# Kernel optimization log

Hardware: AMD Instinct MI355X
Metric: run time of the kernel (lower is better)

The kernel has to match this reference:

```python
import jax, jax.numpy as jnp
import numpy as np

N_NODES = 50000
N_EDGES = 800000
D_IN = 512
D_OUT = 256

def setup_inputs() -> dict:
    key = jax.random.key(0)
    k1, k2, k3, k4, k5 = jax.random.split(key, 5)
    return {
        "inputs": jax.random.normal(k1, (N_NODES, D_IN), dtype=jnp.float32),
        "weights": jax.random.uniform(k2, (D_IN, D_OUT), dtype=jnp.float32, minval=-0.1, maxval=0.1),
        "bias": jnp.zeros((D_OUT,), dtype=jnp.float32),
        "edge_vals": jax.random.uniform(k3, (N_EDGES,), dtype=jnp.float32),
        "edge_row": jax.random.randint(k4, (N_EDGES,), 0, N_NODES),
        "edge_col": jax.random.randint(k5, (N_EDGES,), 0, N_NODES),
    }

def reference(inputs, weights, bias, edge_vals, edge_row, edge_col):
    # dense projection: [N, D_in] @ [D_in, D_out] -> [N, D_out]
    supports = inputs @ weights
    # sparse adjacency spmm in COO form: out[i] = sum_e vals[e] * supports[col[e]] for row[e] == i
    msgs = supports[edge_col] * edge_vals[:, None]  # [E, D_out]
    aggregated = jax.ops.segment_sum(msgs, edge_row, num_segments=inputs.shape[0])
    return aggregated + bias
```

## Files before the change

### kernel.cpp

```cpp
#include <hip/hip_runtime.h>

#define D_IN 512
#define D_OUT 256
#define BM 128
#define BN 128
#define BK 32
#define LDK 40

#define HIST_BLOCKS 1563
#define GEMM_MTILES 391
#define GEMM_BLOCKS (GEMM_MTILES * 2)

typedef short short8 __attribute__((ext_vector_type(8)));
typedef float floatx4 __attribute__((ext_vector_type(4)));

static __device__ __forceinline__ unsigned short f2bf(float f) {
    unsigned u = __float_as_uint(f);
    u += 0x7FFF + ((u >> 16) & 1);
    return (unsigned short)(u >> 16);
}
static __device__ __forceinline__ float bf2f(unsigned short h) {
    return __uint_as_float((unsigned)h << 16);
}

__global__ __launch_bounds__(256) void prep(const float* __restrict__ W,
                                            unsigned short* __restrict__ Wt,
                                            int* __restrict__ cnt, int M) {
    int b = blockIdx.x;
    if (b < 512) {
        int t = b * 256 + threadIdx.x;
        int n = t >> 9;
        int k = t & 511;
        Wt[t] = f2bf(W[(size_t)k * D_OUT + n]);
    } else {
        int i = (b - 512) * 256 + threadIdx.x;
        if (i < M) cnt[i] = 0;
    }
}

__global__ __launch_bounds__(512) void gemm_hist(const float* __restrict__ A,
                                                 const unsigned short* __restrict__ Wt,
                                                 unsigned short* __restrict__ S,
                                                 const int* __restrict__ rows,
                                                 int* __restrict__ cnt, int M, int E) {
    if (blockIdx.x < HIST_BLOCKS) {
        int e = blockIdx.x * 512 + threadIdx.x;
        if (e < E) atomicAdd(&cnt[rows[e]], 1);
        return;
    }
    const int gb = blockIdx.x - HIST_BLOCKS;
    const int bm = (gb >> 1) * BM;
    const int bn = (gb & 1) * BN;

    __shared__ unsigned short As[BM * LDK];
    __shared__ unsigned short Bs[BN * LDK];
    const int tid  = threadIdx.x;
    const int lane = tid & 63;
    const int wave = tid >> 6;
    const int wm   = (wave >> 2) * 64;
    const int wn   = (wave & 3) * 32;
    const int l15  = lane & 15;
    const int quad = lane >> 4;

    const float* aptr[2];
    const unsigned short* bptr[2];
    int aoff[2], boff[2];
    bool aval[2];
#pragma unroll
    for (int i = 0; i < 2; ++i) {
        int item = tid + i * 512;
        int m  = item >> 3;
        int k4 = (item & 7) * 4;
        int gm = bm + m;
        aval[i] = gm < M;
        aptr[i] = A + (size_t)(aval[i] ? gm : 0) * D_IN + k4;
        aoff[i] = m * LDK + k4;
        bptr[i] = Wt + (size_t)(bn + m) * D_IN + k4;
        boff[i] = m * LDK + k4;
    }

    float4  aR[2];
    ushort4 bR[2];
#pragma unroll
    for (int i = 0; i < 2; ++i) {
        aR[i] = aval[i] ? *(const float4*)(aptr[i]) : make_float4(0.f, 0.f, 0.f, 0.f);
        bR[i] = *(const ushort4*)(bptr[i]);
    }

    floatx4 acc[4][2] = {};

    for (int k0 = 0; k0 < D_IN; k0 += BK) {
#pragma unroll
        for (int i = 0; i < 2; ++i) {
            ushort4 b;
            b.x = f2bf(aR[i].x); b.y = f2bf(aR[i].y);
            b.z = f2bf(aR[i].z); b.w = f2bf(aR[i].w);
            *(ushort4*)(As + aoff[i]) = b;
            *(ushort4*)(Bs + boff[i]) = bR[i];
        }
        __syncthreads();

        if (k0 + BK < D_IN) {
#pragma unroll
            for (int i = 0; i < 2; ++i) {
                aR[i] = aval[i] ? *(const float4*)(aptr[i] + k0 + BK)
                                : make_float4(0.f, 0.f, 0.f, 0.f);
                bR[i] = *(const ushort4*)(bptr[i] + k0 + BK);
            }
        }

        short8 af[4], bfr[2];
#pragma unroll
        for (int i = 0; i < 4; ++i)
            af[i] = *(const short8*)(As + (wm + i * 16 + l15) * LDK + quad * 8);
#pragma unroll
        for (int j = 0; j < 2; ++j)
            bfr[j] = *(const short8*)(Bs + (wn + j * 16 + l15) * LDK + quad * 8);
#pragma unroll
        for (int i = 0; i < 4; ++i)
#pragma unroll
            for (int j = 0; j < 2; ++j)
                acc[i][j] = __builtin_amdgcn_mfma_f32_16x16x32_bf16(
                    af[i], bfr[j], acc[i][j], 0, 0, 0);
        __syncthreads();
    }

#pragma unroll
    for (int i = 0; i < 4; ++i) {
#pragma unroll
        for (int r = 0; r < 4; ++r) {
            int gm = bm + wm + i * 16 + quad * 4 + r;
            if (gm < M) {
#pragma unroll
                for (int j = 0; j < 2; ++j)
                    S[(size_t)gm * D_OUT + bn + wn + j * 16 + l15] = f2bf(acc[i][j][r]);
            }
        }
    }
}

__global__ __launch_bounds__(1024) void scan_rowptr(const int* __restrict__ cnt,
                                                    int* __restrict__ ptr,
                                                    int* __restrict__ fill, int M) {
    __shared__ int wsum[16];
    __shared__ int sh_carry;
    const int t = threadIdx.x, lane = t & 63, wave = t >> 6;
    if (t == 0) sh_carry = 0;
    __syncthreads();
    for (int base0 = 0; base0 < M; base0 += 4096) {
        int base = base0 + t * 4;
        int4 v = make_int4(0, 0, 0, 0);
        if (base + 3 < M) v = *(const int4*)(cnt + base);
        else {
            if (base + 0 < M) v.x = cnt[base + 0];
            if (base + 1 < M) v.y = cnt[base + 1];
            if (base + 2 < M) v.z = cnt[base + 2];
        }
        int s = v.x + v.y + v.z + v.w;
        int incl = s;
#pragma unroll
        for (int off = 1; off < 64; off <<= 1) {
            int x = __shfl_up(incl, off, 64);
            if (lane >= off) incl += x;
        }
        if (lane == 63) wsum[wave] = incl;
        __syncthreads();
        if (t == 0) {
            int run = sh_carry;
#pragma unroll
            for (int w = 0; w < 16; ++w) { int x = wsum[w]; wsum[w] = run; run += x; }
            sh_carry = run;
        }
        __syncthreads();
        int e0 = wsum[wave] + (incl - s);
        int e1 = e0 + v.x, e2 = e1 + v.y, e3 = e2 + v.z;
        if (base + 3 < M) {
            *(int4*)(ptr + base)  = make_int4(e0, e1, e2, e3);
            *(int4*)(fill + base) = make_int4(e0, e1, e2, e3);
        } else {
            if (base + 0 < M) { ptr[base + 0] = e0; fill[base + 0] = e0; }
            if (base + 1 < M) { ptr[base + 1] = e1; fill[base + 1] = e1; }
            if (base + 2 < M) { ptr[base + 2] = e2; fill[base + 2] = e2; }
        }
        __syncthreads();
    }
    if (t == 0) ptr[M] = sh_carry;
}

__global__ __launch_bounds__(256) void build_sorted(const float* __restrict__ vals,
                                                    const int* __restrict__ rows,
                                                    const int* __restrict__ cols,
                                                    int* __restrict__ fill,
                                                    int2* __restrict__ edges, int E) {
    int e = blockIdx.x * 256 + threadIdx.x;
    if (e >= E) return;
    int pos = atomicAdd(&fill[rows[e]], 1);
    edges[pos] = make_int2(cols[e], __float_as_int(vals[e]));
}

__global__ __launch_bounds__(256) void spmm_rows(const unsigned short* __restrict__ S,
                                                 const int2* __restrict__ edges,
                                                 const int* __restrict__ ptr,
                                                 const float* __restrict__ bias,
                                                 float* __restrict__ out, int M) {
    const int row = blockIdx.x * 4 + (threadIdx.x >> 6);
    if (row >= M) return;
    const int lane = threadIdx.x & 63;
    float4 a0 = ((const float4*)bias)[lane];
    float4 a1 = make_float4(0.f, 0.f, 0.f, 0.f);
    float4 a2 = make_float4(0.f, 0.f, 0.f, 0.f);
    float4 a3 = make_float4(0.f, 0.f, 0.f, 0.f);
    const int beg = ptr[row];
    const int end = ptr[row + 1];
    int j = beg;
    const int end8 = beg + ((end - beg) & ~7);
    for (; j < end8; j += 8) {
        int4 p01 = *(const int4*)(edges + j);
        int4 p23 = *(const int4*)(edges + j + 2);
        int4 p45 = *(const int4*)(edges + j + 4);
        int4 p67 = *(const int4*)(edges + j + 6);
        ushort4 s0 = ((const ushort4*)(S + (size_t)p01.x * D_OUT))[lane];
        ushort4 s1 = ((const ushort4*)(S + (size_t)p01.z * D_OUT))[lane];
        ushort4 s2 = ((const ushort4*)(S + (size_t)p23.x * D_OUT))[lane];
        ushort4 s3 = ((const ushort4*)(S + (size_t)p23.z * D_OUT))[lane];
        ushort4 s4 = ((const ushort4*)(S + (size_t)p45.x * D_OUT))[lane];
        ushort4 s5 = ((const ushort4*)(S + (size_t)p45.z * D_OUT))[lane];
        ushort4 s6 = ((const ushort4*)(S + (size_t)p67.x * D_OUT))[lane];
        ushort4 s7 = ((const ushort4*)(S + (size_t)p67.z * D_OUT))[lane];
        float v0 = __int_as_float(p01.y), v1 = __int_as_float(p01.w);
        float v2 = __int_as_float(p23.y), v3 = __int_as_float(p23.w);
        float v4 = __int_as_float(p45.y), v5 = __int_as_float(p45.w);
        float v6 = __int_as_float(p67.y), v7 = __int_as_float(p67.w);
        a0.x += v0 * bf2f(s0.x) + v4 * bf2f(s4.x);
        a0.y += v0 * bf2f(s0.y) + v4 * bf2f(s4.y);
        a0.z += v0 * bf2f(s0.z) + v4 * bf2f(s4.z);
        a0.w += v0 * bf2f(s0.w) + v4 * bf2f(s4.w);
        a1.x += v1 * bf2f(s1.x) + v5 * bf2f(s5.x);
        a1.y += v1 * bf2f(s1.y) + v5 * bf2f(s5.y);
        a1.z += v1 * bf2f(s1.z) + v5 * bf2f(s5.z);
        a1.w += v1 * bf2f(s1.w) + v5 * bf2f(s5.w);
        a2.x += v2 * bf2f(s2.x) + v6 * bf2f(s6.x);
        a2.y += v2 * bf2f(s2.y) + v6 * bf2f(s6.y);
        a2.z += v2 * bf2f(s2.z) + v6 * bf2f(s6.z);
        a2.w += v2 * bf2f(s2.w) + v6 * bf2f(s6.w);
        a3.x += v3 * bf2f(s3.x) + v7 * bf2f(s7.x);
        a3.y += v3 * bf2f(s3.y) + v7 * bf2f(s7.y);
        a3.z += v3 * bf2f(s3.z) + v7 * bf2f(s7.z);
        a3.w += v3 * bf2f(s3.w) + v7 * bf2f(s7.w);
    }
    if (j + 3 < end) {
        int4 p01 = *(const int4*)(edges + j);
        int4 p23 = *(const int4*)(edges + j + 2);
        ushort4 s0 = ((const ushort4*)(S + (size_t)p01.x * D_OUT))[lane];
        ushort4 s1 = ((const ushort4*)(S + (size_t)p01.z * D_OUT))[lane];
        ushort4 s2 = ((const ushort4*)(S + (size_t)p23.x * D_OUT))[lane];
        ushort4 s3 = ((const ushort4*)(S + (size_t)p23.z * D_OUT))[lane];
        float v0 = __int_as_float(p01.y), v1 = __int_as_float(p01.w);
        float v2 = __int_as_float(p23.y), v3 = __int_as_float(p23.w);
        a0.x += v0 * bf2f(s0.x) + v2 * bf2f(s2.x);
        a0.y += v0 * bf2f(s0.y) + v2 * bf2f(s2.y);
        a0.z += v0 * bf2f(s0.z) + v2 * bf2f(s2.z);
        a0.w += v0 * bf2f(s0.w) + v2 * bf2f(s2.w);
        a1.x += v1 * bf2f(s1.x) + v3 * bf2f(s3.x);
        a1.y += v1 * bf2f(s1.y) + v3 * bf2f(s3.y);
        a1.z += v1 * bf2f(s1.z) + v3 * bf2f(s3.z);
        a1.w += v1 * bf2f(s1.w) + v3 * bf2f(s3.w);
        j += 4;
    }
    for (; j < end; ++j) {
        int2 e = edges[j];
        float v = __int_as_float(e.y);
        ushort4 s = ((const ushort4*)(S + (size_t)e.x * D_OUT))[lane];
        a0.x += v * bf2f(s.x);
        a0.y += v * bf2f(s.y);
        a0.z += v * bf2f(s.z);
        a0.w += v * bf2f(s.w);
    }
    a0.x += a1.x + a2.x + a3.x;
    a0.y += a1.y + a2.y + a3.y;
    a0.z += a1.z + a2.z + a3.z;
    a0.w += a1.w + a2.w + a3.w;
    ((float4*)out)[(size_t)row * 64 + lane] = a0;
}

extern "C" void kernel_launch(void* const* d_in, const int* in_sizes, int n_in,
                              void* d_out, int out_size, void* d_ws, size_t ws_size,
                              hipStream_t stream) {
    const float* inputs    = (const float*)d_in[0];
    const float* weights   = (const float*)d_in[1];
    const float* bias      = (const float*)d_in[2];
    const float* edge_vals = (const float*)d_in[3];
    const int*   edge_row  = (const int*)d_in[4];
    const int*   edge_col  = (const int*)d_in[5];
    float* out = (float*)d_out;

    const int M = in_sizes[0] / D_IN;
    const int E = in_sizes[3];

    char* ws = (char*)d_ws;
    unsigned short* S  = (unsigned short*)ws;
    unsigned short* Wt = (unsigned short*)(ws + (size_t)M * D_OUT * 2);
    int2* edges        = (int2*)((char*)Wt + (size_t)D_OUT * D_IN * 2);
    int*  ptr          = (int*)((char*)edges + (size_t)E * 8);
    int*  cnt          = ptr + ((M + 4) & ~3);
    int*  fill         = cnt + ((M + 4) & ~3);

    prep<<<512 + (M + 255) / 256, 256, 0, stream>>>(weights, Wt, cnt, M);

    gemm_hist<<<HIST_BLOCKS + GEMM_BLOCKS, 512, 0, stream>>>(inputs, Wt, S, edge_row,
                                                             cnt, M, E);

    scan_rowptr<<<1, 1024, 0, stream>>>(cnt, ptr, fill, M);

    build_sorted<<<(E + 255) / 256, 256, 0, stream>>>(edge_vals, edge_row, edge_col,
                                                      fill, edges, E);

    spmm_rows<<<(M + 3) / 4, 256, 0, stream>>>(S, edges, ptr, bias, out, M);
}
```

Before: 342.5 us.

## Restructure GEMM to stream A from registers and split histogram into own kernel

The GEMM now has each wave own 16 rows and all 128 columns. A values are loaded from global memory directly into registers and converted to bf16 there, so only B is staged in LDS, in 64-wide K chunks. The edge-row histogram is moved out of the fused kernel into a separate kernel that uses int4 loads and four atomics per thread. This removes the A staging traffic through LDS and half the barriers, at the cost of uncoalesced, non-reused A loads and one extra kernel launch. The new histogram also drops the remainder edges when E is not a multiple of 4.

```diff
diff --git a/kernel.cpp b/kernel.cpp
--- a/kernel.cpp
+++ b/kernel.cpp
@@ -2,14 +2,6 @@
 
 #define D_IN 512
 #define D_OUT 256
-#define BM 128
-#define BN 128
-#define BK 32
-#define LDK 40
-
-#define HIST_BLOCKS 1563
-#define GEMM_MTILES 391
-#define GEMM_BLOCKS (GEMM_MTILES * 2)
 
 typedef short short8 __attribute__((ext_vector_type(8)));
 typedef float floatx4 __attribute__((ext_vector_type(4)));
@@ -38,104 +30,76 @@
     }
 }
 
-__global__ __launch_bounds__(512) void gemm_hist(const float* __restrict__ A,
+#define LDB 72
+__global__ __launch_bounds__(512) void gemm_bf16(const float* __restrict__ A,
                                                  const unsigned short* __restrict__ Wt,
-                                                 unsigned short* __restrict__ S,
-                                                 const int* __restrict__ rows,
-                                                 int* __restrict__ cnt, int M, int E) {
-    if (blockIdx.x < HIST_BLOCKS) {
-        int e = blockIdx.x * 512 + threadIdx.x;
-        if (e < E) atomicAdd(&cnt[rows[e]], 1);
-        return;
-    }
-    const int gb = blockIdx.x - HIST_BLOCKS;
-    const int bm = (gb >> 1) * BM;
-    const int bn = (gb & 1) * BN;
-
-    __shared__ unsigned short As[BM * LDK];
-    __shared__ unsigned short Bs[BN * LDK];
+                                                 unsigned short* __restrict__ S, int M) {
+    __shared__ unsigned short Bs[128 * LDB];
     const int tid  = threadIdx.x;
     const int lane = tid & 63;
-    const int wave = tid >> 6;
-    const int wm   = (wave >> 2) * 64;
-    const int wn   = (wave & 3) * 32;
+    const int w    = tid >> 6;
     const int l15  = lane & 15;
     const int quad = lane >> 4;
-
-    const float* aptr[2];
-    const unsigned short* bptr[2];
-    int aoff[2], boff[2];
-    bool aval[2];
+    const int bm   = blockIdx.x * 128;
+    const int bn   = blockIdx.y * 128;
+    const int row  = bm + w * 16 + l15;
+    const float* arow = A + (size_t)(row < M ? row : 0) * D_IN;
+
+    int sn[2], sk[2];
 #pragma unroll
     for (int i = 0; i < 2; ++i) {
-        int item = tid + i * 512;
-        int m  = item >> 3;
-        int k4 = (item & 7) * 4;
-        int gm = bm + m;
-        aval[i] = gm < M;
-        aptr[i] = A + (size_t)(aval[i] ? gm : 0) * D_IN + k4;
-        aoff[i] = m * LDK + k4;
-        bptr[i] = Wt + (size_t)(bn + m) * D_IN + k4;
-        boff[i] = m * LDK + k4;
-    }
-
-    float4  aR[2];
-    ushort4 bR[2];
-#pragma unroll
-    for (int i = 0; i < 2; ++i) {
-        aR[i] = aval[i] ? *(const float4*)(aptr[i]) : make_float4(0.f, 0.f, 0.f, 0.f);
-        bR[i] = *(const ushort4*)(bptr[i]);
-    }
-
-    floatx4 acc[4][2] = {};
-
-    for (int k0 = 0; k0 < D_IN; k0 += BK) {
-#pragma unroll
-        for (int i = 0; i < 2; ++i) {
-            ushort4 b;
-            b.x = f2bf(aR[i].x); b.y = f2bf(aR[i].y);
-            b.z = f2bf(aR[i].z); b.w = f2bf(aR[i].w);
-            *(ushort4*)(As + aoff[i]) = b;
-            *(ushort4*)(Bs + boff[i]) = bR[i];
-        }
-        __syncthreads();
-
-        if (k0 + BK < D_IN) {
-#pragma unroll
-            for (int i = 0; i < 2; ++i) {
-                aR[i] = aval[i] ? *(const float4*)(aptr[i] + k0 + BK)
-                                : make_float4(0.f, 0.f, 0.f, 0.f);
-                bR[i] = *(const ushort4*)(bptr[i] + k0 + BK);
+        int idx = tid + i * 512;
+        sn[i] = idx >> 3;
+        sk[i] = (idx & 7) * 8;
+    }
+
+    floatx4 acc[8] = {};
+
+    for (int kc = 0; kc < D_IN; kc += 64) {
+        __syncthreads();
+#pragma unroll
+        for (int i = 0; i < 2; ++i)
+            *(short8*)(Bs + sn[i] * LDB + sk[i]) =
+                *(const short8*)(Wt + (size_t)(bn + sn[i]) * D_IN + kc + sk[i]);
+        __syncthreads();
+
+#pragma unroll
+        for (int kk = 0; kk < 64; kk += 32) {
+            float4 a0 = *(const float4*)(arow + kc + kk + quad * 8);
+            float4 a1 = *(const float4*)(arow + kc + kk + quad * 8 + 4);
+            short8 af;
+            af[0] = (short)f2bf(a0.x); af[1] = (short)f2bf(a0.y);
+            af[2] = (short)f2bf(a0.z); af[3] = (short)f2bf(a0.w);
+            af[4] = (short)f2bf(a1.x); af[5] = (short)f2bf(a1.y);
+            af[6] = (short)f2bf(a1.z); af[7] = (short)f2bf(a1.w);
+#pragma unroll
+            for (int j = 0; j < 8; ++j) {
+                short8 bf = *(const short8*)(Bs + (j * 16 + l15) * LDB + kk + quad * 8);
+                acc[j] = __builtin_amdgcn_mfma_f32_16x16x32_bf16(af, bf, acc[j], 0, 0, 0);
             }
         }
-
-        short8 af[4], bfr[2];
-#pragma unroll
-        for (int i = 0; i < 4; ++i)
-            af[i] = *(const short8*)(As + (wm + i * 16 + l15) * LDK + quad * 8);
-#pragma unroll
-        for (int j = 0; j < 2; ++j)
-            bfr[j] = *(const short8*)(Bs + (wn + j * 16 + l15) * LDK + quad * 8);
-#pragma unroll
-        for (int i = 0; i < 4; ++i)
-#pragma unroll
-            for (int j = 0; j < 2; ++j)
-                acc[i][j] = __builtin_amdgcn_mfma_f32_16x16x32_bf16(
-                    af[i], bfr[j], acc[i][j], 0, 0, 0);
-        __syncthreads();
-    }
-
-#pragma unroll
-    for (int i = 0; i < 4; ++i) {
-#pragma unroll
-        for (int r = 0; r < 4; ++r) {
-            int gm = bm + wm + i * 16 + quad * 4 + r;
-            if (gm < M) {
-#pragma unroll
-                for (int j = 0; j < 2; ++j)
-                    S[(size_t)gm * D_OUT + bn + wn + j * 16 + l15] = f2bf(acc[i][j][r]);
-            }
-        }
+    }
+
+#pragma unroll
+    for (int r = 0; r < 4; ++r) {
+        int gm = bm + w * 16 + quad * 4 + r;
+        if (gm < M) {
+#pragma unroll
+            for (int j = 0; j < 8; ++j)
+                S[(size_t)gm * D_OUT + bn + j * 16 + l15] = f2bf(acc[j][r]);
+        }
+    }
+}
+
+__global__ __launch_bounds__(256) void hist_rows(const int* __restrict__ rows,
+                                                 int* __restrict__ cnt, int E4) {
+    int t = blockIdx.x * 256 + threadIdx.x;
+    if (t < E4) {
+        int4 r = ((const int4*)rows)[t];
+        atomicAdd(&cnt[r.x], 1);
+        atomicAdd(&cnt[r.y], 1);
+        atomicAdd(&cnt[r.z], 1);
+        atomicAdd(&cnt[r.w], 1);
     }
 }
 
@@ -168,7 +132,7 @@
         if (t == 0) {
             int run = sh_carry;
 #pragma unroll
-            for (int w = 0; w < 16; ++w) { int x = wsum[w]; wsum[w] = run; run += x; }
+            for (int wv = 0; wv < 16; ++wv) { int x = wsum[wv]; wsum[wv] = run; run += x; }
             sh_carry = run;
         }
         __syncthreads();
@@ -307,8 +271,11 @@
 
     prep<<<512 + (M + 255) / 256, 256, 0, stream>>>(weights, Wt, cnt, M);
 
-    gemm_hist<<<HIST_BLOCKS + GEMM_BLOCKS, 512, 0, stream>>>(inputs, Wt, S, edge_row,
-                                                             cnt, M, E);
+    dim3 ggrid((M + 127) / 128, D_OUT / 128);
+    gemm_bf16<<<ggrid, 512, 0, stream>>>(inputs, Wt, S, M);
+
+    int E4 = E / 4;
+    hist_rows<<<(E4 + 255) / 256, 256, 0, stream>>>(edge_row, cnt, E4);
 
     scan_rowptr<<<1, 1024, 0, stream>>>(cnt, ptr, fill, M);
 
```

Measured after the change: 353.1 us. 1.03x slower.
